# Kernel tuning notes

Measured on AMD Instinct MI355X. Metric: run time of the kernel, lower is better.

The kernel has to match this reference:

```python
import jax, jax.numpy as jnp
import numpy as np

DIM = 768
NUM_HEADS = 12
HEAD_DIM = DIM // NUM_HEADS
SCALE = HEAD_DIM ** -0.5


def setup_inputs() -> dict:
    key = jax.random.key(0)
    k1, k2, k3 = jax.random.split(key, 3)
    B, N = 4, 2048
    x = jax.random.normal(k1, (B, N, DIM), dtype=jnp.float32)
    qkv_w = jax.random.normal(k2, (3 * DIM, DIM), dtype=jnp.float32) * (DIM ** -0.5)
    proj_w = jax.random.normal(k3, (DIM, DIM), dtype=jnp.float32) * (DIM ** -0.5)
    proj_b = jnp.zeros((DIM,), dtype=jnp.float32)
    return {"x": x, "qkv_w": qkv_w, "proj_w": proj_w, "proj_b": proj_b}


def reference(x, qkv_w, proj_w, proj_b):
    B, N, C = x.shape
    # qkv projection (no bias; qkv_bias=False)
    qkv = jnp.einsum('bnc,dc->bnd', x, qkv_w)               # [B,N,3C]
    qkv = qkv.reshape(B, N, 3, NUM_HEADS, HEAD_DIM)
    qkv = jnp.transpose(qkv, (2, 0, 3, 1, 4))               # [3,B,H,N,Dh]
    q, k, v = qkv[0] * SCALE, qkv[1], qkv[2]
    attn = jnp.einsum('bhqd,bhkd->bhqk', q, k)              # [B,H,N,N]
    attn = jax.nn.softmax(attn, axis=-1)
    out = jnp.einsum('bhqk,bhkd->bhqd', attn, v)            # [B,H,N,Dh]
    out = jnp.transpose(out, (0, 2, 1, 3)).reshape(B, N, C)
    out = jnp.einsum('bnc,dc->bnd', out, proj_w) + proj_b
    return out
```

## Files before the change

kernel.cpp:

```cpp
#include <hip/hip_runtime.h>
#include <cstdint>
#include <cstddef>

typedef __attribute__((ext_vector_type(8))) short short8v;
typedef __attribute__((ext_vector_type(4))) float f32x4;
typedef __attribute__((ext_vector_type(16))) float f32x16;
typedef __attribute__((ext_vector_type(4))) unsigned int u32x4;
typedef unsigned short us;

#define GLL16(gsrc, ldst)                                                           \
  __builtin_amdgcn_global_load_lds((__attribute__((address_space(1))) void*)(gsrc), \
                                   (__attribute__((address_space(3))) void*)(ldst), \
                                   16, 0, 0)

#define WAITV4()  asm volatile("s_waitcnt vmcnt(4)" ::: "memory")
#define WAITV0()  asm volatile("s_waitcnt vmcnt(0)" ::: "memory")
#define BARRIER() do { __builtin_amdgcn_s_barrier(); asm volatile("" ::: "memory"); } while (0)
#define MFMA32(a, b, c) __builtin_amdgcn_mfma_f32_32x32x16_bf16((a), (b), (c), 0, 0, 0)

static __device__ __forceinline__ us f2bf(float f) {
  unsigned int u = __float_as_uint(f);
  u += 0x7FFFu + ((u >> 16) & 1u);
  return (us)(u >> 16);
}

static __device__ __forceinline__ unsigned int cvtpk_bf16(float lo, float hi) {
  unsigned int r;
  asm("v_cvt_pk_bf16_f32 %0, %1, %2" : "=v"(r) : "v"(lo), "v"(hi));
  return r;
}

template <int B>
static __device__ __forceinline__ short8v pack_swap(const f32x16& p) {
  unsigned int X = cvtpk_bf16(p[B + 0], p[B + 1]);
  unsigned int Y = cvtpk_bf16(p[B + 2], p[B + 3]);
  unsigned int Z = cvtpk_bf16(p[B + 4], p[B + 5]);
  unsigned int W = cvtpk_bf16(p[B + 6], p[B + 7]);
  asm("v_permlane32_swap_b32 %0, %1" : "+v"(X), "+v"(Z));
  asm("v_permlane32_swap_b32 %0, %1" : "+v"(Y), "+v"(W));
  u32x4 f;
  f.x = X; f.y = Y; f.z = Z; f.w = W;
  return __builtin_bit_cast(short8v, f);
}

__global__ void cvt_all(const float4* __restrict__ i0, ushort4* __restrict__ o0, int n0,
                        const float4* __restrict__ i1, ushort4* __restrict__ o1, int n1,
                        const float4* __restrict__ i2, ushort4* __restrict__ o2, int n2)
{
  int i = blockIdx.x * 256 + threadIdx.x;
  const float4* src;
  ushort4* dst;
  if (i < n0)            { src = i0;      dst = o0; }
  else if (i < n0 + n1)  { i -= n0;       src = i1; dst = o1; }
  else if (i < n0+n1+n2) { i -= n0 + n1;  src = i2; dst = o2; }
  else return;
  float4 v = src[i];
  dst[i] = make_ushort4(f2bf(v.x), f2bf(v.y), f2bf(v.z), f2bf(v.w));
}

template <int EPI>
__global__ __launch_bounds__(256, 3)
void gemm_pipe(const us* __restrict__ A, const us* __restrict__ Bw,
               int M, int N, int K,
               us* __restrict__ qout, us* __restrict__ kout, us* __restrict__ vtout,
               const float* __restrict__ bias, float* __restrict__ fout)
{
  __shared__ us SH[3][2][128 * 32];

  const int tid  = threadIdx.x;
  const int lane = tid & 63;
  const int w    = tid >> 6;
  const int g    = lane >> 4;
  const int c    = lane & 15;
  const int wr   = w >> 1;
  const int wc   = w & 1;
  const int ntn  = N >> 7;

  const int nwg  = (M >> 7) * ntn;
  const int cpx  = nwg >> 3;
  const int bid  = (blockIdx.x & 7) * cpx + (blockIdx.x >> 3);
  const int tm   = bid / ntn;
  const int tn   = bid - tm * ntn;
  const int row_a0 = tm * 128;
  const int col_b0 = tn * 128;

  f32x4 acc[4][4];
#pragma unroll
  for (int i = 0; i < 4; ++i)
#pragma unroll
    for (int j = 0; j < 4; ++j) acc[i][j] = (f32x4){0.f, 0.f, 0.f, 0.f};

#define STAGE_AB(buf, ks)                                                  \
  do {                                                                     \
    _Pragma("unroll")                                                      \
    for (int p = 0; p < 2; ++p) {                                          \
      int G = p * 256 + tid;                                               \
      int kslot = G >> 7, row = G & 127;                                   \
      GLL16(A + (size_t)(row_a0 + row) * K + (ks) * 32 + kslot * 8,        \
            &SH[buf][0][G * 8]);                                           \
    }                                                                      \
    _Pragma("unroll")                                                      \
    for (int p = 0; p < 2; ++p) {                                          \
      int G = p * 256 + tid;                                               \
      int kslot = G >> 7, row = G & 127;                                   \
      GLL16(Bw + (size_t)(col_b0 + row) * K + (ks) * 32 + kslot * 8,       \
            &SH[buf][1][G * 8]);                                           \
    }                                                                      \
  } while (0)

  const int nt = K >> 5;
  STAGE_AB(0, 0);
  STAGE_AB(1, 1);
  WAITV4();
  BARRIER();

  for (int t = 0; t < nt; ++t) {
    const int cur = t % 3;
    if (t + 2 < nt) STAGE_AB((t + 2) % 3, t + 2);

    short8v af[4], bfr[4];
#pragma unroll
    for (int mi = 0; mi < 4; ++mi)
      af[mi] = *(const short8v*)&SH[cur][0][(g * 128 + wr * 64 + mi * 16 + c) * 8];
#pragma unroll
    for (int nj = 0; nj < 4; ++nj)
      bfr[nj] = *(const short8v*)&SH[cur][1][(g * 128 + wc * 64 + nj * 16 + c) * 8];
    __builtin_amdgcn_s_setprio(1);
#pragma unroll
    for (int mi = 0; mi < 4; ++mi)
#pragma unroll
      for (int nj = 0; nj < 4; ++nj)
        acc[mi][nj] = __builtin_amdgcn_mfma_f32_16x16x32_bf16(af[mi], bfr[nj], acc[mi][nj], 0, 0, 0);
    __builtin_amdgcn_s_setprio(0);

    if (t + 2 < nt)       WAITV4();
    else if (t + 1 < nt)  WAITV0();
    BARRIER();
  }
#undef STAGE_AB

  const int rbase = row_a0 + wr * 64;
  const int cbase = col_b0 + wc * 64;
  if (EPI == 0) {
    if (cbase < 1536) {
#pragma unroll
      for (int mi = 0; mi < 4; ++mi)
#pragma unroll
        for (int nj = 0; nj < 4; ++nj)
#pragma unroll
          for (int r = 0; r < 4; ++r) {
            float v   = acc[mi][nj][r];
            int mrow  = rbase + mi * 16 + g * 4 + r;
            int d     = cbase + nj * 16 + c;
            int hh    = d < 768 ? (d >> 6) : ((d - 768) >> 6);
            int dh    = d & 63;
            int b     = mrow >> 11, n = mrow & 2047;
            size_t bh = (size_t)(b * 12 + hh);
            if (d < 768) qout[(bh * 2048 + n) * 64 + dh] = f2bf(v * 0.18033688f);
            else         kout[(bh * 2048 + n) * 64 + dh] = f2bf(v);
          }
    } else {
      us* Lw = &SH[0][0][0] + w * (64 * 72);
#pragma unroll
      for (int mi = 0; mi < 4; ++mi)
#pragma unroll
        for (int nj = 0; nj < 4; ++nj)
#pragma unroll
          for (int r = 0; r < 4; ++r)
            Lw[(nj * 16 + c) * 72 + mi * 16 + g * 4 + r] = f2bf(acc[mi][nj][r]);
      const int b   = rbase >> 11;
      const int nl0 = rbase & 2047;
      const int h2  = (cbase - 1536) >> 6;
      const size_t vrow0 = ((size_t)(b * 12 + h2)) * 64;
#pragma unroll
      for (int p = 0; p < 8; ++p) {
        int G   = p * 64 + lane;
        int dl  = G >> 3;
        int seg = G & 7;
        short8v vv = *(const short8v*)&Lw[dl * 72 + seg * 8];
        *(short8v*)(vtout + (vrow0 + dl) * 2048 + nl0 + seg * 8) = vv;
      }
    }
  } else {
#pragma unroll
    for (int mi = 0; mi < 4; ++mi)
#pragma unroll
      for (int nj = 0; nj < 4; ++nj) {
        int d = cbase + nj * 16 + c;
        float bv = bias[d];
#pragma unroll
        for (int r = 0; r < 4; ++r) {
          int mrow = rbase + mi * 16 + g * 4 + r;
          fout[(size_t)mrow * N + d] = acc[mi][nj][r] + bv;
        }
      }
  }
}

__global__ __launch_bounds__(256, 3)
void attn_fwd(const us* __restrict__ Qg, const us* __restrict__ Kg,
              const us* __restrict__ Vg, us* __restrict__ Og)
{
  __shared__ us Ks[2][8 * 64 * 8];
  __shared__ us Vs[2][8 * 64 * 8];

  const int tid  = threadIdx.x;
  const int lane = tid & 63;
  const int w    = tid >> 6;
  const int q31  = lane & 31;
  const int hi   = lane >> 5;

  const int lin = blockIdx.x;
  const int xcd = lin & 7;
  const int idx = lin >> 3;
  const int bh  = xcd * 6 + (idx >> 4);
  const int qt  = idx & 15;
  const int b   = bh / 12;
  const int h   = bh - b * 12;

  const size_t qrow0 = (size_t)bh * 2048 + qt * 128 + w * 32;

  short8v qf[4];
#pragma unroll
  for (int dc = 0; dc < 4; ++dc)
    qf[dc] = *(const short8v*)(Qg + (qrow0 + q31) * 64 + dc * 16 + hi * 8);

  short8v ones;
#pragma unroll
  for (int j = 0; j < 8; ++j) ones[j] = (short)0x3F80;

  f32x16 o0, o1, ls, z16;
#pragma unroll
  for (int r = 0; r < 16; ++r) { o0[r] = 0.f; o1[r] = 0.f; ls[r] = 0.f; z16[r] = 0.f; }

  const size_t kbase = (size_t)bh * 2048 * 64;
  const size_t vbase = (size_t)bh * 64 * 2048;

#define STAGE_KV(buf, kv0)                                             \
  do {                                                                 \
    _Pragma("unroll")                                                  \
    for (int p = 0; p < 2; ++p) {                                      \
      int G = p * 256 + tid;                                           \
      int kslot = G >> 6, row = G & 63;                                \
      GLL16(Kg + kbase + (size_t)((kv0) + row) * 64 + kslot * 8,       \
            &Ks[buf][(p * 256 + w * 64) * 8]);                         \
    }                                                                  \
    _Pragma("unroll")                                                  \
    for (int p = 0; p < 2; ++p) {                                      \
      int G = p * 256 + tid;                                           \
      int kvslot = G >> 6, dh = G & 63;                                \
      GLL16(Vg + vbase + (size_t)dh * 2048 + (kv0) + kvslot * 8,       \
            &Vs[buf][(p * 256 + w * 64) * 8]);                         \
    }                                                                  \
  } while (0)

  STAGE_KV(0, 0);
  __syncthreads();

  for (int t = 0; t < 32; ++t) {
    const int cur = t & 1;
    if (t < 31) STAGE_KV(cur ^ 1, (t + 1) * 64);

    f32x16 s0, s1;
    __builtin_amdgcn_s_setprio(1);
    {
      const us* kb = &Ks[cur][(hi * 64 + q31) * 8];
      short8v kf0 = *(const short8v*)kb;
      short8v kf1 = *(const short8v*)(kb + 32 * 8);
      s0 = MFMA32(kf0, qf[0], z16);
      s1 = MFMA32(kf1, qf[0], z16);
    }
#pragma unroll
    for (int dc = 1; dc < 4; ++dc) {
      const us* kb = &Ks[cur][((dc * 2 + hi) * 64 + q31) * 8];
      short8v kf0 = *(const short8v*)kb;
      short8v kf1 = *(const short8v*)(kb + 32 * 8);
      s0 = MFMA32(kf0, qf[dc], s0);
      s1 = MFMA32(kf1, qf[dc], s1);
    }
    __builtin_amdgcn_s_setprio(0);

#pragma unroll
    for (int r = 0; r < 16; ++r) {
      s0[r] = __builtin_amdgcn_exp2f(s0[r]);
      s1[r] = __builtin_amdgcn_exp2f(s1[r]);
    }

    short8v pa[4];
    pa[0] = pack_swap<0>(s0);
    pa[1] = pack_swap<8>(s0);
    pa[2] = pack_swap<0>(s1);
    pa[3] = pack_swap<8>(s1);

    __builtin_amdgcn_s_setprio(1);
#pragma unroll
    for (int kc = 0; kc < 4; ++kc) {
      const us* vb = &Vs[cur][((kc * 2 + hi) * 64 + q31) * 8];
      short8v vf0 = *(const short8v*)vb;
      short8v vf1 = *(const short8v*)(vb + 32 * 8);
      o0 = MFMA32(pa[kc], vf0, o0);
      o1 = MFMA32(pa[kc], vf1, o1);
      ls = MFMA32(pa[kc], ones, ls);
    }
    __builtin_amdgcn_s_setprio(0);

    __syncthreads();
  }
#undef STAGE_KV

  const int n0w = qt * 128 + w * 32;
#pragma unroll
  for (int r = 0; r < 16; ++r) {
    float iv = 1.0f / ls[r];
    int n = n0w + (r & 3) + 8 * (r >> 2) + 4 * hi;
    size_t rowbase = ((size_t)b * 2048 + n) * 768 + h * 64 + q31;
    Og[rowbase]      = f2bf(o0[r] * iv);
    Og[rowbase + 32] = f2bf(o1[r] * iv);
  }
}

extern "C" void kernel_launch(void* const* d_in, const int* in_sizes, int n_in,
                              void* d_out, int out_size, void* d_ws, size_t ws_size,
                              hipStream_t stream)
{
  const float* x      = (const float*)d_in[0];
  const float* qkv_w  = (const float*)d_in[1];
  const float* proj_w = (const float*)d_in[2];
  const float* proj_b = (const float*)d_in[3];

  char* ws = (char*)d_ws;
  const size_t SZ_X    = (size_t)8192 * 768 * 2;
  const size_t SZ_WQKV = (size_t)2304 * 768 * 2;
  const size_t SZ_WP   = (size_t)768 * 768 * 2;
  const size_t SZ_HEAD = (size_t)48 * 2048 * 64;

  us* x_bf   = (us*)(ws);
  us* wqkv   = (us*)(ws + SZ_X);
  us* wproj  = (us*)(ws + SZ_X + SZ_WQKV);
  us* q_bf   = (us*)(ws + SZ_X + SZ_WQKV + SZ_WP);
  us* k_bf   = q_bf + SZ_HEAD;
  us* vt_bf  = k_bf + SZ_HEAD;
  us* attn_o = x_bf;

  const int n0 = 8192 * 768 / 4, n1 = 2304 * 768 / 4, n2 = 768 * 768 / 4;
  cvt_all<<<(n0 + n1 + n2 + 255) / 256, 256, 0, stream>>>(
      (const float4*)x, (ushort4*)x_bf, n0,
      (const float4*)qkv_w, (ushort4*)wqkv, n1,
      (const float4*)proj_w, (ushort4*)wproj, n2);

  gemm_pipe<0><<<64 * 18, 256, 0, stream>>>(x_bf, wqkv, 8192, 2304, 768,
                                            q_bf, k_bf, vt_bf, nullptr, nullptr);

  attn_fwd<<<768, 256, 0, stream>>>(q_bf, k_bf, vt_bf, attn_o);

  gemm_pipe<1><<<64 * 6, 256, 0, stream>>>(attn_o, wproj, 8192, 768, 768,
                                           nullptr, nullptr, nullptr, proj_b, (float*)d_out);
}
```

Before: 176.4 us.

## Process two 32-row query tiles per wave in attention with 128-thread blocks

The attention kernel now runs 2 waves per block instead of 4, and each wave handles 64 query rows as two 32-row sub-tiles that share every K and V fragment read from LDS. This halves LDS reads per MFMA and gives each wave more independent MFMA chains to interleave. The cost is higher register pressure from doubled accumulators and Q fragments, fewer waves per block loading each KV tile, and a changed occupancy target in the launch bounds.

```diff
diff --git a/kernel.cpp b/kernel.cpp
--- a/kernel.cpp
+++ b/kernel.cpp
@@ -197,7 +197,7 @@
   }
 }
 
-__global__ __launch_bounds__(256, 3)
+__global__ __launch_bounds__(128, 2)
 void attn_fwd(const us* __restrict__ Qg, const us* __restrict__ Kg,
               const us* __restrict__ Vg, us* __restrict__ Og)
 {
@@ -205,8 +205,8 @@
   __shared__ us Vs[2][8 * 64 * 8];
 
   const int tid  = threadIdx.x;
+  const int w    = tid >> 6;
   const int lane = tid & 63;
-  const int w    = tid >> 6;
   const int q31  = lane & 31;
   const int hi   = lane >> 5;
 
@@ -218,20 +218,26 @@
   const int b   = bh / 12;
   const int h   = bh - b * 12;
 
-  const size_t qrow0 = (size_t)bh * 2048 + qt * 128 + w * 32;
-
-  short8v qf[4];
-#pragma unroll
-  for (int dc = 0; dc < 4; ++dc)
-    qf[dc] = *(const short8v*)(Qg + (qrow0 + q31) * 64 + dc * 16 + hi * 8);
+  const size_t qrowA = (size_t)bh * 2048 + qt * 128 + w * 64;
+  const size_t qrowB = qrowA + 32;
+
+  short8v qfA[4], qfB[4];
+#pragma unroll
+  for (int dc = 0; dc < 4; ++dc) {
+    qfA[dc] = *(const short8v*)(Qg + (qrowA + q31) * 64 + dc * 16 + hi * 8);
+    qfB[dc] = *(const short8v*)(Qg + (qrowB + q31) * 64 + dc * 16 + hi * 8);
+  }
 
   short8v ones;
 #pragma unroll
   for (int j = 0; j < 8; ++j) ones[j] = (short)0x3F80;
 
-  f32x16 o0, o1, ls, z16;
-#pragma unroll
-  for (int r = 0; r < 16; ++r) { o0[r] = 0.f; o1[r] = 0.f; ls[r] = 0.f; z16[r] = 0.f; }
+  f32x16 oA0, oA1, oB0, oB1, lsA, lsB, z16;
+#pragma unroll
+  for (int r = 0; r < 16; ++r) {
+    oA0[r] = 0.f; oA1[r] = 0.f; oB0[r] = 0.f; oB1[r] = 0.f;
+    lsA[r] = 0.f; lsB[r] = 0.f; z16[r] = 0.f;
+  }
 
   const size_t kbase = (size_t)bh * 2048 * 64;
   const size_t vbase = (size_t)bh * 64 * 2048;
@@ -239,18 +245,18 @@
 #define STAGE_KV(buf, kv0)                                             \
   do {                                                                 \
     _Pragma("unroll")                                                  \
-    for (int p = 0; p < 2; ++p) {                                      \
-      int G = p * 256 + tid;                                           \
+    for (int p = 0; p < 4; ++p) {                                      \
+      int G = p * 128 + tid;                                           \
       int kslot = G >> 6, row = G & 63;                                \
       GLL16(Kg + kbase + (size_t)((kv0) + row) * 64 + kslot * 8,       \
-            &Ks[buf][(p * 256 + w * 64) * 8]);                         \
+            &Ks[buf][(p * 128 + w * 64) * 8]);                         \
     }                                                                  \
     _Pragma("unroll")                                                  \
-    for (int p = 0; p < 2; ++p) {                                      \
-      int G = p * 256 + tid;                                           \
+    for (int p = 0; p < 4; ++p) {                                      \
+      int G = p * 128 + tid;                                           \
       int kvslot = G >> 6, dh = G & 63;                                \
       GLL16(Vg + vbase + (size_t)dh * 2048 + (kv0) + kvslot * 8,       \
-            &Vs[buf][(p * 256 + w * 64) * 8]);                         \
+            &Vs[buf][(p * 128 + w * 64) * 8]);                         \
     }                                                                  \
   } while (0)
 
@@ -261,36 +267,42 @@
     const int cur = t & 1;
     if (t < 31) STAGE_KV(cur ^ 1, (t + 1) * 64);
 
-    f32x16 s0, s1;
+    f32x16 sA0, sA1, sB0, sB1;
     __builtin_amdgcn_s_setprio(1);
     {
       const us* kb = &Ks[cur][(hi * 64 + q31) * 8];
       short8v kf0 = *(const short8v*)kb;
       short8v kf1 = *(const short8v*)(kb + 32 * 8);
-      s0 = MFMA32(kf0, qf[0], z16);
-      s1 = MFMA32(kf1, qf[0], z16);
+      sA0 = MFMA32(kf0, qfA[0], z16);
+      sA1 = MFMA32(kf1, qfA[0], z16);
+      sB0 = MFMA32(kf0, qfB[0], z16);
+      sB1 = MFMA32(kf1, qfB[0], z16);
     }
 #pragma unroll
     for (int dc = 1; dc < 4; ++dc) {
       const us* kb = &Ks[cur][((dc * 2 + hi) * 64 + q31) * 8];
       short8v kf0 = *(const short8v*)kb;
       short8v kf1 = *(const short8v*)(kb + 32 * 8);
-      s0 = MFMA32(kf0, qf[dc], s0);
-      s1 = MFMA32(kf1, qf[dc], s1);
+      sA0 = MFMA32(kf0, qfA[dc], sA0);
+      sA1 = MFMA32(kf1, qfA[dc], sA1);
+      sB0 = MFMA32(kf0, qfB[dc], sB0);
+      sB1 = MFMA32(kf1, qfB[dc], sB1);
     }
     __builtin_amdgcn_s_setprio(0);
 
 #pragma unroll
     for (int r = 0; r < 16; ++r) {
-      s0[r] = __builtin_amdgcn_exp2f(s0[r]);
-      s1[r] = __builtin_amdgcn_exp2f(s1[r]);
-    }
-
-    short8v pa[4];
-    pa[0] = pack_swap<0>(s0);
-    pa[1] = pack_swap<8>(s0);
-    pa[2] = pack_swap<0>(s1);
-    pa[3] = pack_swap<8>(s1);
+      sA0[r] = __builtin_amdgcn_exp2f(sA0[r]);
+      sA1[r] = __builtin_amdgcn_exp2f(sA1[r]);
+      sB0[r] = __builtin_amdgcn_exp2f(sB0[r]);
+      sB1[r] = __builtin_amdgcn_exp2f(sB1[r]);
+    }
+
+    short8v paA[4], paB[4];
+    paA[0] = pack_swap<0>(sA0);  paA[1] = pack_swap<8>(sA0);
+    paA[2] = pack_swap<0>(sA1);  paA[3] = pack_swap<8>(sA1);
+    paB[0] = pack_swap<0>(sB0);  paB[1] = pack_swap<8>(sB0);
+    paB[2] = pack_swap<0>(sB1);  paB[3] = pack_swap<8>(sB1);
 
     __builtin_amdgcn_s_setprio(1);
 #pragma unroll
@@ -298,9 +310,12 @@
       const us* vb = &Vs[cur][((kc * 2 + hi) * 64 + q31) * 8];
       short8v vf0 = *(const short8v*)vb;
       short8v vf1 = *(const short8v*)(vb + 32 * 8);
-      o0 = MFMA32(pa[kc], vf0, o0);
-      o1 = MFMA32(pa[kc], vf1, o1);
-      ls = MFMA32(pa[kc], ones, ls);
+      oA0 = MFMA32(paA[kc], vf0, oA0);
+      oA1 = MFMA32(paA[kc], vf1, oA1);
+      lsA = MFMA32(paA[kc], ones, lsA);
+      oB0 = MFMA32(paB[kc], vf0, oB0);
+      oB1 = MFMA32(paB[kc], vf1, oB1);
+      lsB = MFMA32(paB[kc], ones, lsB);
     }
     __builtin_amdgcn_s_setprio(0);
 
@@ -308,14 +323,18 @@
   }
 #undef STAGE_KV
 
-  const int n0w = qt * 128 + w * 32;
+  const int nA = qt * 128 + w * 64;
 #pragma unroll
   for (int r = 0; r < 16; ++r) {
-    float iv = 1.0f / ls[r];
-    int n = n0w + (r & 3) + 8 * (r >> 2) + 4 * hi;
-    size_t rowbase = ((size_t)b * 2048 + n) * 768 + h * 64 + q31;
-    Og[rowbase]      = f2bf(o0[r] * iv);
-    Og[rowbase + 32] = f2bf(o1[r] * iv);
+    int crow = (r & 3) + 8 * (r >> 2) + 4 * hi;
+    float ivA = 1.0f / lsA[r];
+    size_t rbA = ((size_t)b * 2048 + nA + crow) * 768 + h * 64 + q31;
+    Og[rbA]      = f2bf(oA0[r] * ivA);
+    Og[rbA + 32] = f2bf(oA1[r] * ivA);
+    float ivB = 1.0f / lsB[r];
+    size_t rbB = rbA + (size_t)32 * 768;
+    Og[rbB]      = f2bf(oB0[r] * ivB);
+    Og[rbB + 32] = f2bf(oB1[r] * ivB);
   }
 }
 
@@ -351,7 +370,7 @@
   gemm_pipe<0><<<64 * 18, 256, 0, stream>>>(x_bf, wqkv, 8192, 2304, 768,
                                             q_bf, k_bf, vt_bf, nullptr, nullptr);
 
-  attn_fwd<<<768, 256, 0, stream>>>(q_bf, k_bf, vt_bf, attn_o);
+  attn_fwd<<<768, 128, 0, stream>>>(q_bf, k_bf, vt_bf, attn_o);
 
   gemm_pipe<1><<<64 * 6, 256, 0, stream>>>(attn_o, wproj, 8192, 768, 768,
                                            nullptr, nullptr, nullptr, proj_b, (float*)d_out);
```

Result: slower. 188.0 us (+6.6%).

## Split QKV GEMM into dedicated 256x128-tile kernel with 8 waves

Applied to the files above, without the earlier changes.

Adds a dedicated QKV projection kernel that uses 256x128 output tiles with 512 threads (8 waves) and double buffering in place of the old 3-stage 128x128 pipeline. The aim is more reuse of the shared B tile and fewer workgroups. The V-transpose epilogue now runs in two passes through a smaller padded LDS scratch. The output projection keeps the old kernel, renamed and with the QKV epilogue removed. The risks are a shallower pipeline, since the loop waits for all loads to finish every iteration, and higher register and LDS pressure per block.

```diff
diff --git a/kernel.cpp b/kernel.cpp
--- a/kernel.cpp
+++ b/kernel.cpp
@@ -58,11 +58,133 @@
   dst[i] = make_ushort4(f2bf(v.x), f2bf(v.y), f2bf(v.z), f2bf(v.w));
 }
 
-template <int EPI>
+__global__ __launch_bounds__(512, 4)
+void gemm_qkv(const us* __restrict__ A, const us* __restrict__ Bw,
+              int M, int N, int K,
+              us* __restrict__ qout, us* __restrict__ kout, us* __restrict__ vtout)
+{
+  __shared__ us SH[2][12288];
+
+  const int tid  = threadIdx.x;
+  const int lane = tid & 63;
+  const int w    = tid >> 6;
+  const int g    = lane >> 4;
+  const int c    = lane & 15;
+  const int wr   = w >> 1;
+  const int wc   = w & 1;
+  const int ntn  = N >> 7;
+
+  const int nwg  = (M >> 8) * ntn;
+  const int cpx  = nwg >> 3;
+  const int bid  = (blockIdx.x & 7) * cpx + (blockIdx.x >> 3);
+  const int tm   = bid / ntn;
+  const int tn   = bid - tm * ntn;
+  const int row_a0 = tm * 256;
+  const int col_b0 = tn * 128;
+
+  f32x4 acc[4][4];
+#pragma unroll
+  for (int i = 0; i < 4; ++i)
+#pragma unroll
+    for (int j = 0; j < 4; ++j) acc[i][j] = (f32x4){0.f, 0.f, 0.f, 0.f};
+
+#define STAGE_AB(buf, ks)                                                  \
+  do {                                                                     \
+    _Pragma("unroll")                                                      \
+    for (int p = 0; p < 2; ++p) {                                          \
+      int G = p * 512 + tid;                                               \
+      int kslot = G >> 8, row = G & 255;                                   \
+      GLL16(A + (size_t)(row_a0 + row) * K + (ks) * 32 + kslot * 8,        \
+            &SH[buf][G * 8]);                                              \
+    }                                                                      \
+    {                                                                      \
+      int G = tid;                                                         \
+      int kslot = G >> 7, row = G & 127;                                   \
+      GLL16(Bw + (size_t)(col_b0 + row) * K + (ks) * 32 + kslot * 8,       \
+            &SH[buf][8192 + G * 8]);                                       \
+    }                                                                      \
+  } while (0)
+
+  const int nt = K >> 5;
+  STAGE_AB(0, 0);
+  WAITV0();
+  BARRIER();
+
+  for (int t = 0; t < nt; ++t) {
+    const int cur = t & 1;
+    if (t + 1 < nt) STAGE_AB(cur ^ 1, t + 1);
+
+    short8v af[4], bfr[4];
+#pragma unroll
+    for (int mi = 0; mi < 4; ++mi)
+      af[mi] = *(const short8v*)&SH[cur][(g * 256 + wr * 64 + mi * 16 + c) * 8];
+#pragma unroll
+    for (int nj = 0; nj < 4; ++nj)
+      bfr[nj] = *(const short8v*)&SH[cur][8192 + (g * 128 + wc * 64 + nj * 16 + c) * 8];
+    __builtin_amdgcn_s_setprio(1);
+#pragma unroll
+    for (int mi = 0; mi < 4; ++mi)
+#pragma unroll
+      for (int nj = 0; nj < 4; ++nj)
+        acc[mi][nj] = __builtin_amdgcn_mfma_f32_16x16x32_bf16(af[mi], bfr[nj], acc[mi][nj], 0, 0, 0);
+    __builtin_amdgcn_s_setprio(0);
+
+    WAITV0();
+    BARRIER();
+  }
+#undef STAGE_AB
+
+  const int rbase = row_a0 + wr * 64;
+  const int cbase = col_b0 + wc * 64;
+  if (cbase < 1536) {
+#pragma unroll
+    for (int mi = 0; mi < 4; ++mi)
+#pragma unroll
+      for (int nj = 0; nj < 4; ++nj)
+#pragma unroll
+        for (int r = 0; r < 4; ++r) {
+          float v   = acc[mi][nj][r];
+          int mrow  = rbase + mi * 16 + g * 4 + r;
+          int d     = cbase + nj * 16 + c;
+          int hh    = d < 768 ? (d >> 6) : ((d - 768) >> 6);
+          int dh    = d & 63;
+          int b     = mrow >> 11, n = mrow & 2047;
+          size_t bh = (size_t)(b * 12 + hh);
+          if (d < 768) qout[(bh * 2048 + n) * 64 + dh] = f2bf(v * 0.18033688f);
+          else         kout[(bh * 2048 + n) * 64 + dh] = f2bf(v);
+        }
+  } else {
+    us* Lw = &SH[0][0] + w * (64 * 40);
+    const int b   = rbase >> 11;
+    const int nl0 = rbase & 2047;
+    const int h2  = (cbase - 1536) >> 6;
+    const size_t vrow0 = ((size_t)(b * 12 + h2)) * 64;
+#pragma unroll
+    for (int pass = 0; pass < 2; ++pass) {
+#pragma unroll
+      for (int mi2 = 0; mi2 < 2; ++mi2) {
+        int mi = pass * 2 + mi2;
+#pragma unroll
+        for (int nj = 0; nj < 4; ++nj)
+#pragma unroll
+          for (int r = 0; r < 4; ++r)
+            Lw[(nj * 16 + c) * 40 + mi2 * 16 + g * 4 + r] = f2bf(acc[mi][nj][r]);
+      }
+#pragma unroll
+      for (int p = 0; p < 4; ++p) {
+        int G   = p * 64 + lane;
+        int dl  = G >> 2;
+        int seg = G & 3;
+        short8v vv = *(const short8v*)&Lw[dl * 40 + seg * 8];
+        *(short8v*)(vtout + (vrow0 + dl) * 2048 + nl0 + pass * 32 + seg * 8) = vv;
+      }
+    }
+  }
+}
+
 __global__ __launch_bounds__(256, 3)
-void gemm_pipe(const us* __restrict__ A, const us* __restrict__ Bw,
+void gemm_proj(const us* __restrict__ A, const us* __restrict__ Bw,
                int M, int N, int K,
-               us* __restrict__ qout, us* __restrict__ kout, us* __restrict__ vtout,
                const float* __restrict__ bias, float* __restrict__ fout)
 {
   __shared__ us SH[3][2][128 * 32];
@@ -141,60 +263,18 @@
 
   const int rbase = row_a0 + wr * 64;
   const int cbase = col_b0 + wc * 64;
-  if (EPI == 0) {
-    if (cbase < 1536) {
-#pragma unroll
-      for (int mi = 0; mi < 4; ++mi)
-#pragma unroll
-        for (int nj = 0; nj < 4; ++nj)
-#pragma unroll
-          for (int r = 0; r < 4; ++r) {
-            float v   = acc[mi][nj][r];
-            int mrow  = rbase + mi * 16 + g * 4 + r;
-            int d     = cbase + nj * 16 + c;
-            int hh    = d < 768 ? (d >> 6) : ((d - 768) >> 6);
-            int dh    = d & 63;
-            int b     = mrow >> 11, n = mrow & 2047;
-            size_t bh = (size_t)(b * 12 + hh);
-            if (d < 768) qout[(bh * 2048 + n) * 64 + dh] = f2bf(v * 0.18033688f);
-            else         kout[(bh * 2048 + n) * 64 + dh] = f2bf(v);
-          }
-    } else {
-      us* Lw = &SH[0][0][0] + w * (64 * 72);
-#pragma unroll
-      for (int mi = 0; mi < 4; ++mi)
-#pragma unroll
-        for (int nj = 0; nj < 4; ++nj)
-#pragma unroll
-          for (int r = 0; r < 4; ++r)
-            Lw[(nj * 16 + c) * 72 + mi * 16 + g * 4 + r] = f2bf(acc[mi][nj][r]);
-      const int b   = rbase >> 11;
-      const int nl0 = rbase & 2047;
-      const int h2  = (cbase - 1536) >> 6;
-      const size_t vrow0 = ((size_t)(b * 12 + h2)) * 64;
-#pragma unroll
-      for (int p = 0; p < 8; ++p) {
-        int G   = p * 64 + lane;
-        int dl  = G >> 3;
-        int seg = G & 7;
-        short8v vv = *(const short8v*)&Lw[dl * 72 + seg * 8];
-        *(short8v*)(vtout + (vrow0 + dl) * 2048 + nl0 + seg * 8) = vv;
+#pragma unroll
+  for (int mi = 0; mi < 4; ++mi)
+#pragma unroll
+    for (int nj = 0; nj < 4; ++nj) {
+      int d = cbase + nj * 16 + c;
+      float bv = bias[d];
+#pragma unroll
+      for (int r = 0; r < 4; ++r) {
+        int mrow = rbase + mi * 16 + g * 4 + r;
+        fout[(size_t)mrow * N + d] = acc[mi][nj][r] + bv;
       }
     }
-  } else {
-#pragma unroll
-    for (int mi = 0; mi < 4; ++mi)
-#pragma unroll
-      for (int nj = 0; nj < 4; ++nj) {
-        int d = cbase + nj * 16 + c;
-        float bv = bias[d];
-#pragma unroll
-        for (int r = 0; r < 4; ++r) {
-          int mrow = rbase + mi * 16 + g * 4 + r;
-          fout[(size_t)mrow * N + d] = acc[mi][nj][r] + bv;
-        }
-      }
-  }
 }
 
 __global__ __launch_bounds__(256, 3)
@@ -348,11 +428,11 @@
       (const float4*)qkv_w, (ushort4*)wqkv, n1,
       (const float4*)proj_w, (ushort4*)wproj, n2);
 
-  gemm_pipe<0><<<64 * 18, 256, 0, stream>>>(x_bf, wqkv, 8192, 2304, 768,
-                                            q_bf, k_bf, vt_bf, nullptr, nullptr);
+  gemm_qkv<<<576, 512, 0, stream>>>(x_bf, wqkv, 8192, 2304, 768,
+                                    q_bf, k_bf, vt_bf);
 
   attn_fwd<<<768, 256, 0, stream>>>(q_bf, k_bf, vt_bf, attn_o);
 
-  gemm_pipe<1><<<64 * 6, 256, 0, stream>>>(attn_o, wproj, 8192, 768, 768,
-                                           nullptr, nullptr, nullptr, proj_b, (float*)d_out);
-}
+  gemm_proj<<<64 * 6, 256, 0, stream>>>(attn_o, wproj, 8192, 768, 768,
+                                        proj_b, (float*)d_out);
+}
```

Result: slower. 191.5 us (+8.6%).
